# Performance work log

Measured on AMD Instinct MI355X. Metric: run time of the kernel, lower is better.

## Reference

```python
import jax, jax.numpy as jnp
import numpy as np
from jax import lax

I, H, D1 = 130, 10, 20  # input_size, hidden_size, linear1 width


def _gru_last(x, Wih, Whh, bih, bhh):
    """PyTorch-convention GRU (gate order r,z,n); returns last hidden state [B,H]."""
    # Precompute input projections for all timesteps: [B,T,3H]
    xi = jnp.einsum('bti,gi->btg', x, Wih) + bih
    h0 = jnp.zeros((x.shape[0], H), x.dtype)

    def step(h, xt):  # xt: [B,3H]
        gh = h @ Whh.T + bhh  # [B,3H]
        r = jax.nn.sigmoid(xt[:, :H] + gh[:, :H])
        z = jax.nn.sigmoid(xt[:, H:2 * H] + gh[:, H:2 * H])
        n = jnp.tanh(xt[:, 2 * H:] + r * gh[:, 2 * H:])
        h_new = (1.0 - z) * n + z * h
        return h_new, None

    hT, _ = lax.scan(step, h0, jnp.swapaxes(xi, 0, 1))  # scan over time
    return hT


def setup_inputs() -> dict:
    key = jax.random.key(0)
    ks = jax.random.split(key, 12)
    B, T = 2048, 128
    s_ih = 1.0 / np.sqrt(H)
    inp = {
        'ru': jax.random.normal(ks[0], (B, T, I), jnp.float32),
        'en': jax.random.normal(ks[1], (B, T, I), jnp.float32),
        'ru_Wih': jax.random.uniform(ks[2], (3 * H, I), jnp.float32, -s_ih, s_ih),
        'ru_Whh': jax.random.uniform(ks[3], (3 * H, H), jnp.float32, -s_ih, s_ih),
        'ru_bih': jax.random.uniform(ks[4], (3 * H,), jnp.float32, -s_ih, s_ih),
        'ru_bhh': jax.random.uniform(ks[5], (3 * H,), jnp.float32, -s_ih, s_ih),
        'en_Wih': jax.random.uniform(ks[6], (3 * H, I), jnp.float32, -s_ih, s_ih),
        'en_Whh': jax.random.uniform(ks[7], (3 * H, H), jnp.float32, -s_ih, s_ih),
        'en_bih': jax.random.uniform(ks[8], (3 * H,), jnp.float32, -s_ih, s_ih),
        'en_bhh': jax.random.uniform(ks[9], (3 * H,), jnp.float32, -s_ih, s_ih),
        'W1': jax.random.uniform(ks[10], (D1, 2 * H), jnp.float32, -1 / np.sqrt(2 * H), 1 / np.sqrt(2 * H)),
        'b1': jnp.zeros((D1,), jnp.float32),
        'W2': jax.random.uniform(ks[11], (1, D1), jnp.float32, -1 / np.sqrt(D1), 1 / np.sqrt(D1)),
        'b2': jnp.zeros((1,), jnp.float32),
    }
    return inp


def reference(ru, en, ru_Wih, ru_Whh, ru_bih, ru_bhh,
              en_Wih, en_Whh, en_bih, en_bhh, W1, b1, W2, b2):
    ru_h = _gru_last(ru, ru_Wih, ru_Whh, ru_bih, ru_bhh)  # [B,H] (last timestep output)
    en_h = _gru_last(en, en_Wih, en_Whh, en_bih, en_bhh)  # [B,H]
    grus_out = jnp.concatenate([ru_h, en_h], axis=1)       # [B,2H]
    h1 = grus_out @ W1.T + b1                              # [B,20] (no activation in original)
    out = h1 @ W2.T + b2                                   # [B,1]
    return out
```

## Files before the change

### kernel.cpp

```cpp
#include <hip/hip_runtime.h>
#include <hip/hip_bf16.h>


#define BB 2048
#define TT 128
#define II 130
#define ROWS_PER_GRU (BB * TT)
#define ROWS_TOTAL   (2 * ROWS_PER_GRU)

typedef __attribute__((ext_vector_type(8))) short short8v;
typedef __attribute__((ext_vector_type(4))) float f32x4;

__device__ __forceinline__ float sigmoidf_fast(float x) {
    return __fdividef(1.f, 1.f + __expf(-x));
}
__device__ __forceinline__ float tanhf_fast(float x) {
    float ax = fabsf(x);
    float e = __expf(-2.f * ax);
    float t = __fdividef(1.f - e, 1.f + e);
    return copysignf(t, x);
}

__device__ __forceinline__ void split2(float x0, float x1,
                                       unsigned& hi, unsigned& lo) {
    unsigned u0 = __float_as_uint(x0), u1 = __float_as_uint(x1);
    hi = (u0 >> 16) | (u1 & 0xffff0000u);
    float f0 = __uint_as_float(u0 & 0xffff0000u);
    float f1 = __uint_as_float(u1 & 0xffff0000u);
    unsigned l0 = __float_as_uint(x0 - f0);
    unsigned l1 = __float_as_uint(x1 - f1);
    lo = (l0 >> 16) | (l1 & 0xffff0000u);
}

union U8 { unsigned u[4]; short8v v; };

__device__ __forceinline__ void load_split(const float* __restrict__ p,
                                           short8v& hi, short8v& lo) {
    U8 H, L;
    #pragma unroll
    for (int i = 0; i < 4; ++i) {
        const float2 xy = *(const float2*)(p + 2 * i);
        split2(xy.x, xy.y, H.u[i], L.u[i]);
    }
    hi = H.v; lo = L.v;
}

__global__ __launch_bounds__(256)
void xi_gemm(const float* __restrict__ ru, const float* __restrict__ en,
             const float* __restrict__ ruWih, const float* __restrict__ rubih,
             const float* __restrict__ enWih, const float* __restrict__ enbih,
             float* __restrict__ xi)
{
    const int tid  = threadIdx.x;
    const int wv   = tid >> 6;
    const int lane = tid & 63;
    const int lr   = lane & 15;
    const int lk   = lane >> 4;
    const int w    = blockIdx.x * 4 + wv;
    const int gru  = (w >= 4096);
    const long row0 = (long)(w & 4095) * 64;

    const float* __restrict__ X   = gru ? en    : ru;
    const float* __restrict__ Wf  = gru ? enWih : ruWih;
    const float* __restrict__ bih = gru ? enbih : rubih;

    short8v Bhi[2][4], Blo[2][4];
    float biasv[2], wt0[2], wt1[2];
    #pragma unroll
    for (int t = 0; t < 2; ++t) {
        const int g = 16 * t + lr;
        const int gv = (g < 30) ? g : 0;
        #pragma unroll
        for (int q = 0; q < 4; ++q)
            load_split(Wf + (long)gv * II + 32 * q + 8 * lk, Bhi[t][q], Blo[t][q]);
        if (g >= 30) {
            const short8v z = {0, 0, 0, 0, 0, 0, 0, 0};
            #pragma unroll
            for (int q = 0; q < 4; ++q) { Bhi[t][q] = z; Blo[t][q] = z; }
        }
        biasv[t] = bih[gv];
        const float2 wt = *(const float2*)(Wf + (long)gv * II + 128);
        wt0[t] = wt.x; wt1[t] = wt.y;
    }

    __shared__ __align__(16) float lds[4][16 * II];
    float4* __restrict__ L4 = (float4*)lds[wv];
    const float* __restrict__ Lf = lds[wv];

    const float4* __restrict__ src = (const float4*)X + row0 * (II / 2) / 2;

    const long gb = (long)gru * ROWS_PER_GRU;

    float4 pf0, pf1, pf2, pf3, pf4, pf5, pf6, pf7, pft;
    {
        const float4* __restrict__ s = src;
        pf0 = s[lane];        pf1 = s[64 + lane];
        pf2 = s[128 + lane];  pf3 = s[192 + lane];
        pf4 = s[256 + lane];  pf5 = s[320 + lane];
        pf6 = s[384 + lane];  pf7 = s[448 + lane];
        if (lane < 8) pft = s[512 + lane];
    }

    #pragma unroll
    for (int t = 0; t < 4; ++t) {
        L4[lane]       = pf0;  L4[64 + lane]  = pf1;
        L4[128 + lane] = pf2;  L4[192 + lane] = pf3;
        L4[256 + lane] = pf4;  L4[320 + lane] = pf5;
        L4[384 + lane] = pf6;  L4[448 + lane] = pf7;
        if (lane < 8) L4[512 + lane] = pft;

        if (t < 3) {
            const float4* __restrict__ s = src + 520 * (t + 1);
            pf0 = s[lane];        pf1 = s[64 + lane];
            pf2 = s[128 + lane];  pf3 = s[192 + lane];
            pf4 = s[256 + lane];  pf5 = s[320 + lane];
            pf6 = s[384 + lane];  pf7 = s[448 + lane];
            if (lane < 8) pft = s[512 + lane];
        }

        f32x4 a0 = (f32x4){biasv[0], biasv[0], biasv[0], biasv[0]};
        f32x4 a1 = (f32x4){biasv[1], biasv[1], biasv[1], biasv[1]};
        #pragma unroll
        for (int q = 0; q < 4; ++q) {
            short8v ahi, alo;
            load_split(Lf + lr * II + 32 * q + 8 * lk, ahi, alo);
            a0 = __builtin_amdgcn_mfma_f32_16x16x32_bf16(ahi, Bhi[0][q], a0, 0, 0, 0);
            a0 = __builtin_amdgcn_mfma_f32_16x16x32_bf16(ahi, Blo[0][q], a0, 0, 0, 0);
            a0 = __builtin_amdgcn_mfma_f32_16x16x32_bf16(alo, Bhi[0][q], a0, 0, 0, 0);
            a1 = __builtin_amdgcn_mfma_f32_16x16x32_bf16(ahi, Bhi[1][q], a1, 0, 0, 0);
            a1 = __builtin_amdgcn_mfma_f32_16x16x32_bf16(ahi, Blo[1][q], a1, 0, 0, 0);
            a1 = __builtin_amdgcn_mfma_f32_16x16x32_bf16(alo, Bhi[1][q], a1, 0, 0, 0);
        }

        #pragma unroll
        for (int r = 0; r < 4; ++r) {
            const int rowin = 4 * lk + r;
            const float2 xt = *(const float2*)(Lf + rowin * II + 128);
            const long rr = row0 + 16 * t + rowin;
            float* __restrict__ xo = xi + (gb + rr) * 30;
            const float v0 = a0[r] + xt.x * wt0[0] + xt.y * wt1[0];
            xo[lr] = v0;
            if (lr < 14) {
                const float v1 = a1[r] + xt.x * wt0[1] + xt.y * wt1[1];
                xo[16 + lr] = v1;
            }
        }
    }
}

__global__ __launch_bounds__(256, 4)
void gru_scan(const float* __restrict__ xi,
              const float* __restrict__ ruWhh, const float* __restrict__ rubhh,
              const float* __restrict__ enWhh, const float* __restrict__ enbhh,
              const float* __restrict__ W1, const float* __restrict__ b1,
              const float* __restrict__ W2, const float* __restrict__ b2,
              float* __restrict__ out)
{
    const int tid  = threadIdx.x;
    const int wv   = tid >> 6;
    const int lane = tid & 63;
    const int c    = lane >> 5;
    const int k    = lane & 31;
    const int kq   = (k < 10) ? k : 0;
    const int chain = (blockIdx.x * 4 + wv) * 2 + c;
    const int gru   = chain >> 11;
    const int b     = chain & (BB - 1);

    const float* __restrict__ Whh = gru ? enWhh : ruWhh;
    const float* __restrict__ bhh = gru ? enbhh : rubhh;

    float whhR[10], whhZ[10], whhN[10];
    #pragma unroll
    for (int j = 0; j < 10; ++j) {
        whhR[j] = Whh[kq * 10 + j];
        whhZ[j] = Whh[(10 + kq) * 10 + j];
        whhN[j] = Whh[(20 + kq) * 10 + j];
    }
    const float bR = bhh[kq], bZ = bhh[10 + kq], bN = bhh[20 + kq];

    __shared__ __align__(16) float lds[4][32];
    float* __restrict__ H = lds[wv] + c * 16;
    if (k < 12) H[k] = 0.f;
    float hown = 0.f;

    const float* __restrict__ xrow =
        xi + ((long)gru * ROWS_PER_GRU + (long)b * TT) * 30;

    float xR0 = xrow[kq],      xZ0 = xrow[10 + kq],  xN0 = xrow[20 + kq];
    float xR1 = xrow[30 + kq], xZ1 = xrow[40 + kq],  xN1 = xrow[50 + kq];

    for (int t = 0; t < TT; ++t) {
        const float xR = xR0, xZ = xZ0, xN = xN0;
        xR0 = xR1; xZ0 = xZ1; xN0 = xN1;
        {
            const int tn = (t + 2 < TT) ? t + 2 : TT - 1;
            const float* __restrict__ xp = xrow + (long)tn * 30;
            xR1 = xp[kq]; xZ1 = xp[10 + kq]; xN1 = xp[20 + kq];
        }

        const float4 h03 = *(const float4*)(H);
        const float4 h47 = *(const float4*)(H + 4);
        const float2 h89 = *(const float2*)(H + 8);

        float gr = bR, gz = bZ, gn = bN;
        gr = fmaf(whhR[0], h03.x, gr); gz = fmaf(whhZ[0], h03.x, gz); gn = fmaf(whhN[0], h03.x, gn);
        gr = fmaf(whhR[1], h03.y, gr); gz = fmaf(whhZ[1], h03.y, gz); gn = fmaf(whhN[1], h03.y, gn);
        gr = fmaf(whhR[2], h03.z, gr); gz = fmaf(whhZ[2], h03.z, gz); gn = fmaf(whhN[2], h03.z, gn);
        gr = fmaf(whhR[3], h03.w, gr); gz = fmaf(whhZ[3], h03.w, gz); gn = fmaf(whhN[3], h03.w, gn);
        gr = fmaf(whhR[4], h47.x, gr); gz = fmaf(whhZ[4], h47.x, gz); gn = fmaf(whhN[4], h47.x, gn);
        gr = fmaf(whhR[5], h47.y, gr); gz = fmaf(whhZ[5], h47.y, gz); gn = fmaf(whhN[5], h47.y, gn);
        gr = fmaf(whhR[6], h47.z, gr); gz = fmaf(whhZ[6], h47.z, gz); gn = fmaf(whhN[6], h47.z, gn);
        gr = fmaf(whhR[7], h47.w, gr); gz = fmaf(whhZ[7], h47.w, gz); gn = fmaf(whhN[7], h47.w, gn);
        gr = fmaf(whhR[8], h89.x, gr); gz = fmaf(whhZ[8], h89.x, gz); gn = fmaf(whhN[8], h89.x, gn);
        gr = fmaf(whhR[9], h89.y, gr); gz = fmaf(whhZ[9], h89.y, gz); gn = fmaf(whhN[9], h89.y, gn);

        const float r = sigmoidf_fast(xR + gr);
        const float z = sigmoidf_fast(xZ + gz);
        const float n = tanhf_fast(xN + r * gn);
        const float hnew = fmaf(z, hown - n, n);
        hown = hnew;
        if (k < 10) H[k] = hnew;
    }

    float val = 0.f;
    if (k < 10) {
        float v = 0.f;
        #pragma unroll
        for (int d = 0; d < 20; ++d)
            v = fmaf(W2[d], W1[d * 20 + gru * 10 + k], v);
        val = v * hown;
        if (k == 0 && gru == 0) {
            float c0 = b2[0];
            #pragma unroll
            for (int d = 0; d < 20; ++d) c0 = fmaf(W2[d], b1[d], c0);
            val += c0;
        }
    }
    val += __shfl_xor(val, 8);
    val += __shfl_xor(val, 4);
    val += __shfl_xor(val, 2);
    val += __shfl_xor(val, 1);
    if (k == 0) atomicAdd(&out[b], val);
}

__global__ __launch_bounds__(256, 4)
void gru_fused(const float* __restrict__ ru, const float* __restrict__ en,
               const float* __restrict__ ruWih, const float* __restrict__ ruWhh,
               const float* __restrict__ rubih, const float* __restrict__ rubhh,
               const float* __restrict__ enWih, const float* __restrict__ enWhh,
               const float* __restrict__ enbih, const float* __restrict__ enbhh,
               const float* __restrict__ W1, const float* __restrict__ b1,
               const float* __restrict__ W2, const float* __restrict__ b2,
               float* __restrict__ out)
{
    const int tid  = threadIdx.x;
    const int wv   = tid >> 6;
    const int lane = tid & 63;
    const int g    = lane & 31;
    const int h    = lane >> 5;
    const int wid  = blockIdx.x * 4 + wv;
    const int gru  = wid >> 11;
    const int b    = wid & (BB - 1);

    const float* __restrict__ x   = gru ? en    : ru;
    const float* __restrict__ Wih = gru ? enWih : ruWih;
    const float* __restrict__ Whh = gru ? enWhh : ruWhh;
    const float* __restrict__ bih = gru ? enbih : rubih;
    const float* __restrict__ bhh = gru ? enbhh : rubhh;

    __shared__ __align__(16) float lds[4][176];
    float* __restrict__ X    = lds[wv];
    float* __restrict__ PRE  = X + 132;
    float* __restrict__ Hbuf = X + 164;

    const int gq = (g < 30) ? g : 0;
    float wih[64];
    #pragma unroll
    for (int j = 0; j < 64; ++j) wih[j] = Wih[gq * II + h * 64 + j];
    const float w_e = Wih[gq * II + 128 + h];
    float whh[10];
    #pragma unroll
    for (int k = 0; k < 10; ++k) whh[k] = Whh[gq * 10 + k];
    const float bihg = bih[gq];
    const float bhhg = bhh[gq];

    if (lane < 12) Hbuf[lane] = 0.f;
    float hown = 0.f;

    const float* __restrict__ xrow = x + (size_t)b * (TT * II);
    float xa = xrow[lane];
    float xb = xrow[64 + lane];
    float xc = (lane < 2) ? xrow[128 + lane] : 0.f;

    for (int t = 0; t < TT; ++t) {
        X[lane] = xa;
        X[64 + lane] = xb;
        if (lane < 2) X[128 + lane] = xc;
        {
            const int tn = (t < TT - 1) ? t + 1 : t;
            const float* __restrict__ xn = xrow + (size_t)tn * II;
            xa = xn[lane];
            xb = xn[64 + lane];
            xc = (lane < 2) ? xn[128 + lane] : 0.f;
        }
        const float4 h03 = *(const float4*)(Hbuf);
        const float4 h47 = *(const float4*)(Hbuf + 4);
        const float2 h89 = *(const float2*)(Hbuf + 8);
        float gh0 = fmaf(whh[0], h03.x, bhhg);
        float gh1 = whh[1] * h03.y;
        gh0 = fmaf(whh[2], h03.z, gh0);
        gh1 = fmaf(whh[3], h03.w, gh1);
        gh0 = fmaf(whh[4], h47.x, gh0);
        gh1 = fmaf(whh[5], h47.y, gh1);
        gh0 = fmaf(whh[6], h47.z, gh0);
        gh1 = fmaf(whh[7], h47.w, gh1);
        gh0 = fmaf(whh[8], h89.x, gh0);
        gh1 = fmaf(whh[9], h89.y, gh1);
        const float gh = gh0 + gh1;

        float s0 = 0.f, s1 = 0.f, s2 = 0.f, s3 = 0.f;
        const float4* __restrict__ xb4 = (const float4*)(X + h * 64);
        #pragma unroll
        for (int c = 0; c < 16; ++c) {
            const float4 v = xb4[c];
            s0 = fmaf(wih[4 * c + 0], v.x, s0);
            s1 = fmaf(wih[4 * c + 1], v.y, s1);
            s2 = fmaf(wih[4 * c + 2], v.z, s2);
            s3 = fmaf(wih[4 * c + 3], v.w, s3);
        }
        float s = (s0 + s1) + (s2 + s3);
        s = fmaf(w_e, X[128 + h], s);
        s += __shfl_xor(s, 32);

        const float xiv = s + bihg;
        const float pre = xiv + gh;
        if (lane < 30) PRE[lane] = pre;
        const float rpre = PRE[(g - 20) & 31];
        const float zpre = PRE[(g - 10) & 31];
        const float r = sigmoidf_fast(rpre);
        const float z = sigmoidf_fast(zpre);
        const float n = tanhf_fast(xiv + r * gh);
        const float hnew = (1.f - z) * n + z * hown;
        hown = hnew;
        if (lane >= 20 && lane < 30) Hbuf[lane - 20] = hnew;
    }

    float val = 0.f;
    if (lane < 10) {
        const float hk = Hbuf[lane];
        float v = 0.f;
        #pragma unroll
        for (int d = 0; d < 20; ++d)
            v = fmaf(W2[d], W1[d * 20 + gru * 10 + lane], v);
        val = v * hk;
        if (lane == 0 && gru == 0) {
            float c0 = b2[0];
            #pragma unroll
            for (int d = 0; d < 20; ++d) c0 = fmaf(W2[d], b1[d], c0);
            val += c0;
        }
    }
    #pragma unroll
    for (int o = 32; o > 0; o >>= 1) val += __shfl_xor(val, o);
    if (lane == 0) atomicAdd(&out[b], val);
}

extern "C" void kernel_launch(void* const* d_in, const int* in_sizes, int n_in,
                              void* d_out, int out_size, void* d_ws, size_t ws_size,
                              hipStream_t stream) {
    (void)in_sizes; (void)n_in;
    const float* ru    = (const float*)d_in[0];
    const float* en    = (const float*)d_in[1];
    const float* ruWih = (const float*)d_in[2];
    const float* ruWhh = (const float*)d_in[3];
    const float* rubih = (const float*)d_in[4];
    const float* rubhh = (const float*)d_in[5];
    const float* enWih = (const float*)d_in[6];
    const float* enWhh = (const float*)d_in[7];
    const float* enbih = (const float*)d_in[8];
    const float* enbhh = (const float*)d_in[9];
    const float* W1    = (const float*)d_in[10];
    const float* b1    = (const float*)d_in[11];
    const float* W2    = (const float*)d_in[12];
    const float* b2    = (const float*)d_in[13];
    float* out = (float*)d_out;

    hipMemsetAsync(d_out, 0, (size_t)out_size * sizeof(float), stream);

    const size_t xi_bytes = (size_t)ROWS_TOTAL * 30 * sizeof(float);
    if (ws_size >= xi_bytes) {
        float* xi = (float*)d_ws;
        xi_gemm<<<dim3(2048), dim3(256), 0, stream>>>(
            ru, en, ruWih, rubih, enWih, enbih, xi);
        gru_scan<<<dim3(512), dim3(256), 0, stream>>>(
            xi, ruWhh, rubhh, enWhh, enbhh, W1, b1, W2, b2, out);
    } else {
        gru_fused<<<dim3(1024), dim3(256), 0, stream>>>(
            ru, en, ruWih, ruWhh, rubih, rubhh,
            enWih, enWhh, enbih, enbhh, W1, b1, W2, b2, out);
    }
}
```

Before: 118.6 us.

## Shrink xi_gemm tiles to one per wave and broadcast GRU hidden state via shuffles

xi_gemm now has each wave handle a single 16-row tile instead of four pipelined tiles, with four times as many blocks, which gives more parallelism and memory-level concurrency but loses the intra-wave prefetch overlap and reloads the split weights for every tile. In gru_scan the hidden-state exchange through LDS is replaced with ten __shfl broadcasts from lanes in the same half-wave, removing the LDS store/load per timestep. The shuffles are themselves LDS-routed (ds_bpermute) instructions, so they may cost as much as the original vector loads.

```diff
diff --git a/kernel.cpp b/kernel.cpp
--- a/kernel.cpp
+++ b/kernel.cpp
@@ -57,12 +57,24 @@
     const int lr   = lane & 15;
     const int lk   = lane >> 4;
     const int w    = blockIdx.x * 4 + wv;
-    const int gru  = (w >= 4096);
-    const long row0 = (long)(w & 4095) * 64;
+    const int gru  = (w >= 16384);
+    const long row0 = (long)(w & 16383) * 16;
 
     const float* __restrict__ X   = gru ? en    : ru;
     const float* __restrict__ Wf  = gru ? enWih : ruWih;
     const float* __restrict__ bih = gru ? enbih : rubih;
+
+    const float4* __restrict__ src = (const float4*)X + row0 * II / 4;
+    const float4 pf0 = src[lane];
+    const float4 pf1 = src[64 + lane];
+    const float4 pf2 = src[128 + lane];
+    const float4 pf3 = src[192 + lane];
+    const float4 pf4 = src[256 + lane];
+    const float4 pf5 = src[320 + lane];
+    const float4 pf6 = src[384 + lane];
+    const float4 pf7 = src[448 + lane];
+    const float4 pft = (lane < 8) ? src[512 + lane]
+                                  : make_float4(0.f, 0.f, 0.f, 0.f);
 
     short8v Bhi[2][4], Blo[2][4];
     float biasv[2], wt0[2], wt1[2];
@@ -86,64 +98,38 @@
     __shared__ __align__(16) float lds[4][16 * II];
     float4* __restrict__ L4 = (float4*)lds[wv];
     const float* __restrict__ Lf = lds[wv];
-
-    const float4* __restrict__ src = (const float4*)X + row0 * (II / 2) / 2;
+    L4[lane]       = pf0;  L4[64 + lane]  = pf1;
+    L4[128 + lane] = pf2;  L4[192 + lane] = pf3;
+    L4[256 + lane] = pf4;  L4[320 + lane] = pf5;
+    L4[384 + lane] = pf6;  L4[448 + lane] = pf7;
+    if (lane < 8) L4[512 + lane] = pft;
+
+    f32x4 a0 = (f32x4){biasv[0], biasv[0], biasv[0], biasv[0]};
+    f32x4 a1 = (f32x4){biasv[1], biasv[1], biasv[1], biasv[1]};
+    #pragma unroll
+    for (int q = 0; q < 4; ++q) {
+        short8v ahi, alo;
+        load_split(Lf + lr * II + 32 * q + 8 * lk, ahi, alo);
+        a0 = __builtin_amdgcn_mfma_f32_16x16x32_bf16(ahi, Bhi[0][q], a0, 0, 0, 0);
+        a0 = __builtin_amdgcn_mfma_f32_16x16x32_bf16(ahi, Blo[0][q], a0, 0, 0, 0);
+        a0 = __builtin_amdgcn_mfma_f32_16x16x32_bf16(alo, Bhi[0][q], a0, 0, 0, 0);
+        a1 = __builtin_amdgcn_mfma_f32_16x16x32_bf16(ahi, Bhi[1][q], a1, 0, 0, 0);
+        a1 = __builtin_amdgcn_mfma_f32_16x16x32_bf16(ahi, Blo[1][q], a1, 0, 0, 0);
+        a1 = __builtin_amdgcn_mfma_f32_16x16x32_bf16(alo, Bhi[1][q], a1, 0, 0, 0);
+    }
 
     const long gb = (long)gru * ROWS_PER_GRU;
-
-    float4 pf0, pf1, pf2, pf3, pf4, pf5, pf6, pf7, pft;
-    {
-        const float4* __restrict__ s = src;
-        pf0 = s[lane];        pf1 = s[64 + lane];
-        pf2 = s[128 + lane];  pf3 = s[192 + lane];
-        pf4 = s[256 + lane];  pf5 = s[320 + lane];
-        pf6 = s[384 + lane];  pf7 = s[448 + lane];
-        if (lane < 8) pft = s[512 + lane];
-    }
-
-    #pragma unroll
-    for (int t = 0; t < 4; ++t) {
-        L4[lane]       = pf0;  L4[64 + lane]  = pf1;
-        L4[128 + lane] = pf2;  L4[192 + lane] = pf3;
-        L4[256 + lane] = pf4;  L4[320 + lane] = pf5;
-        L4[384 + lane] = pf6;  L4[448 + lane] = pf7;
-        if (lane < 8) L4[512 + lane] = pft;
-
-        if (t < 3) {
-            const float4* __restrict__ s = src + 520 * (t + 1);
-            pf0 = s[lane];        pf1 = s[64 + lane];
-            pf2 = s[128 + lane];  pf3 = s[192 + lane];
-            pf4 = s[256 + lane];  pf5 = s[320 + lane];
-            pf6 = s[384 + lane];  pf7 = s[448 + lane];
-            if (lane < 8) pft = s[512 + lane];
-        }
-
-        f32x4 a0 = (f32x4){biasv[0], biasv[0], biasv[0], biasv[0]};
-        f32x4 a1 = (f32x4){biasv[1], biasv[1], biasv[1], biasv[1]};
-        #pragma unroll
-        for (int q = 0; q < 4; ++q) {
-            short8v ahi, alo;
-            load_split(Lf + lr * II + 32 * q + 8 * lk, ahi, alo);
-            a0 = __builtin_amdgcn_mfma_f32_16x16x32_bf16(ahi, Bhi[0][q], a0, 0, 0, 0);
-            a0 = __builtin_amdgcn_mfma_f32_16x16x32_bf16(ahi, Blo[0][q], a0, 0, 0, 0);
-            a0 = __builtin_amdgcn_mfma_f32_16x16x32_bf16(alo, Bhi[0][q], a0, 0, 0, 0);
-            a1 = __builtin_amdgcn_mfma_f32_16x16x32_bf16(ahi, Bhi[1][q], a1, 0, 0, 0);
-            a1 = __builtin_amdgcn_mfma_f32_16x16x32_bf16(ahi, Blo[1][q], a1, 0, 0, 0);
-            a1 = __builtin_amdgcn_mfma_f32_16x16x32_bf16(alo, Bhi[1][q], a1, 0, 0, 0);
-        }
-
-        #pragma unroll
-        for (int r = 0; r < 4; ++r) {
-            const int rowin = 4 * lk + r;
-            const float2 xt = *(const float2*)(Lf + rowin * II + 128);
-            const long rr = row0 + 16 * t + rowin;
-            float* __restrict__ xo = xi + (gb + rr) * 30;
-            const float v0 = a0[r] + xt.x * wt0[0] + xt.y * wt1[0];
-            xo[lr] = v0;
-            if (lr < 14) {
-                const float v1 = a1[r] + xt.x * wt0[1] + xt.y * wt1[1];
-                xo[16 + lr] = v1;
-            }
+    #pragma unroll
+    for (int r = 0; r < 4; ++r) {
+        const int rowin = 4 * lk + r;
+        const float2 xt = *(const float2*)(Lf + rowin * II + 128);
+        const long rr = row0 + rowin;
+        float* __restrict__ xo = xi + (gb + rr) * 30;
+        const float v0 = a0[r] + xt.x * wt0[0] + xt.y * wt1[0];
+        xo[lr] = v0;
+        if (lr < 14) {
+            const float v1 = a1[r] + xt.x * wt0[1] + xt.y * wt1[1];
+            xo[16 + lr] = v1;
         }
     }
 }
@@ -162,6 +148,7 @@
     const int c    = lane >> 5;
     const int k    = lane & 31;
     const int kq   = (k < 10) ? k : 0;
+    const int base = lane & 32;
     const int chain = (blockIdx.x * 4 + wv) * 2 + c;
     const int gru   = chain >> 11;
     const int b     = chain & (BB - 1);
@@ -178,9 +165,6 @@
     }
     const float bR = bhh[kq], bZ = bhh[10 + kq], bN = bhh[20 + kq];
 
-    __shared__ __align__(16) float lds[4][32];
-    float* __restrict__ H = lds[wv] + c * 16;
-    if (k < 12) H[k] = 0.f;
     float hown = 0.f;
 
     const float* __restrict__ xrow =
@@ -198,28 +182,33 @@
             xR1 = xp[kq]; xZ1 = xp[10 + kq]; xN1 = xp[20 + kq];
         }
 
-        const float4 h03 = *(const float4*)(H);
-        const float4 h47 = *(const float4*)(H + 4);
-        const float2 h89 = *(const float2*)(H + 8);
+        const float h0 = __shfl(hown, base + 0);
+        const float h1 = __shfl(hown, base + 1);
+        const float h2 = __shfl(hown, base + 2);
+        const float h3 = __shfl(hown, base + 3);
+        const float h4 = __shfl(hown, base + 4);
+        const float h5 = __shfl(hown, base + 5);
+        const float h6 = __shfl(hown, base + 6);
+        const float h7 = __shfl(hown, base + 7);
+        const float h8 = __shfl(hown, base + 8);
+        const float h9 = __shfl(hown, base + 9);
 
         float gr = bR, gz = bZ, gn = bN;
-        gr = fmaf(whhR[0], h03.x, gr); gz = fmaf(whhZ[0], h03.x, gz); gn = fmaf(whhN[0], h03.x, gn);
-        gr = fmaf(whhR[1], h03.y, gr); gz = fmaf(whhZ[1], h03.y, gz); gn = fmaf(whhN[1], h03.y, gn);
-        gr = fmaf(whhR[2], h03.z, gr); gz = fmaf(whhZ[2], h03.z, gz); gn = fmaf(whhN[2], h03.z, gn);
-        gr = fmaf(whhR[3], h03.w, gr); gz = fmaf(whhZ[3], h03.w, gz); gn = fmaf(whhN[3], h03.w, gn);
-        gr = fmaf(whhR[4], h47.x, gr); gz = fmaf(whhZ[4], h47.x, gz); gn = fmaf(whhN[4], h47.x, gn);
-        gr = fmaf(whhR[5], h47.y, gr); gz = fmaf(whhZ[5], h47.y, gz); gn = fmaf(whhN[5], h47.y, gn);
-        gr = fmaf(whhR[6], h47.z, gr); gz = fmaf(whhZ[6], h47.z, gz); gn = fmaf(whhN[6], h47.z, gn);
-        gr = fmaf(whhR[7], h47.w, gr); gz = fmaf(whhZ[7], h47.w, gz); gn = fmaf(whhN[7], h47.w, gn);
-        gr = fmaf(whhR[8], h89.x, gr); gz = fmaf(whhZ[8], h89.x, gz); gn = fmaf(whhN[8], h89.x, gn);
-        gr = fmaf(whhR[9], h89.y, gr); gz = fmaf(whhZ[9], h89.y, gz); gn = fmaf(whhN[9], h89.y, gn);
+        gr = fmaf(whhR[0], h0, gr); gz = fmaf(whhZ[0], h0, gz); gn = fmaf(whhN[0], h0, gn);
+        gr = fmaf(whhR[1], h1, gr); gz = fmaf(whhZ[1], h1, gz); gn = fmaf(whhN[1], h1, gn);
+        gr = fmaf(whhR[2], h2, gr); gz = fmaf(whhZ[2], h2, gz); gn = fmaf(whhN[2], h2, gn);
+        gr = fmaf(whhR[3], h3, gr); gz = fmaf(whhZ[3], h3, gz); gn = fmaf(whhN[3], h3, gn);
+        gr = fmaf(whhR[4], h4, gr); gz = fmaf(whhZ[4], h4, gz); gn = fmaf(whhN[4], h4, gn);
+        gr = fmaf(whhR[5], h5, gr); gz = fmaf(whhZ[5], h5, gz); gn = fmaf(whhN[5], h5, gn);
+        gr = fmaf(whhR[6], h6, gr); gz = fmaf(whhZ[6], h6, gz); gn = fmaf(whhN[6], h6, gn);
+        gr = fmaf(whhR[7], h7, gr); gz = fmaf(whhZ[7], h7, gz); gn = fmaf(whhN[7], h7, gn);
+        gr = fmaf(whhR[8], h8, gr); gz = fmaf(whhZ[8], h8, gz); gn = fmaf(whhN[8], h8, gn);
+        gr = fmaf(whhR[9], h9, gr); gz = fmaf(whhZ[9], h9, gz); gn = fmaf(whhN[9], h9, gn);
 
         const float r = sigmoidf_fast(xR + gr);
         const float z = sigmoidf_fast(xZ + gz);
         const float n = tanhf_fast(xN + r * gn);
-        const float hnew = fmaf(z, hown - n, n);
-        hown = hnew;
-        if (k < 10) H[k] = hnew;
+        hown = fmaf(z, hown - n, n);
     }
 
     float val = 0.f;
@@ -390,7 +379,7 @@
     const size_t xi_bytes = (size_t)ROWS_TOTAL * 30 * sizeof(float);
     if (ws_size >= xi_bytes) {
         float* xi = (float*)d_ws;
-        xi_gemm<<<dim3(2048), dim3(256), 0, stream>>>(
+        xi_gemm<<<dim3(8192), dim3(256), 0, stream>>>(
             ru, en, ruWih, rubih, enWih, enbih, xi);
         gru_scan<<<dim3(512), dim3(256), 0, stream>>>(
             xi, ruWhh, rubhh, enWhh, enbhh, W1, b1, W2, b2, out);
```

After: 144.5 us. 1.22x slower.
